# Optimization experiments

Hardware: AMD Instinct MI355X
Metric: run time of the kernel (lower is better)

The kernel has to match this reference:

```python
import jax, jax.numpy as jnp
import numpy as np

NUM_DOMAINS = 8
MARGIN = 1.0


def setup_inputs() -> dict:
    key = jax.random.key(0)
    k1, k2 = jax.random.split(key)
    features = jax.random.normal(k1, (4096, 1024), dtype=jnp.float32)
    domain_labels = jax.random.randint(k2, (4096,), 0, NUM_DOMAINS)
    return {"features": features, "domain_labels": domain_labels}


def reference(features, domain_labels):
    # Full BxB euclidean distance matrix (matches torch.cdist p=2, which uses
    # the mm-based path for this size). Safe sqrt so diagonal zeros are exact.
    sq = jnp.sum(features * features, axis=-1)                      # (B,)
    d2 = sq[:, None] + sq[None, :] - 2.0 * (features @ features.T)  # (B,B)
    d2 = jnp.maximum(d2, 0.0)
    dist = jnp.where(d2 > 0, jnp.sqrt(jnp.where(d2 > 0, d2, 1.0)), 0.0)
    vals = jax.nn.relu(MARGIN - dist)                               # (B,B)

    # Per-domain pair sums via one-hot contraction: s_d = m_d^T V m_d.
    onehot = (domain_labels[:, None] == jnp.arange(NUM_DOMAINS)[None, :]
              ).astype(features.dtype)                              # (B,K)
    n = onehot.sum(axis=0)                                          # (K,)
    row_sums = vals @ onehot                                        # (B,K)
    pair_sums = (onehot * row_sums).sum(axis=0)                     # (K,)

    valid = n > 1  # torch loop skips singleton domains
    per_domain = jnp.where(valid, pair_sums / jnp.maximum(n * n, 1.0), 0.0)
    cnt = valid.sum().astype(features.dtype)
    return jnp.where(cnt > 0, per_domain.sum() / jnp.maximum(cnt, 1.0), 0.0)
```

## Files before the change

### kernel.cpp

```cpp
#include <hip/hip_runtime.h>

#define NDOM 8
#define TT   32
#define KDIM 1024
#define RPAD 1040
#define BMAX 4096
#define GGRID 512

typedef float f32x4 __attribute__((ext_vector_type(4)));

__device__ inline void gload16(const void* g, void* l) {
    __builtin_amdgcn_global_load_lds(
        (const __attribute__((address_space(1))) unsigned int*)g,
        (__attribute__((address_space(3))) unsigned int*)l, 16, 0, 0);
}

__global__ __launch_bounds__(256) void k_prep(
    const float* __restrict__ F, const int* __restrict__ labels, int B,
    unsigned char* __restrict__ Fb, float* __restrict__ sq,
    int* __restrict__ perm, int* __restrict__ dom_off) {
    const int t = threadIdx.x, lane = t & 63, wv = t >> 6;

    if (blockIdx.x == 0) {
        __shared__ int lab[BMAX];
        __shared__ unsigned wcnt[4][NDOM];
        for (int i = t; i < BMAX; i += 256) lab[i] = (i < B) ? labels[i] : -1;
        __syncthreads();

        int nch = (B + 63) >> 6;
        int cpw = (nch + 3) >> 2;
        int c0 = wv * cpw, c1 = min(c0 + cpw, nch);
        unsigned long long below = (1ull << lane) - 1ull;

        unsigned cnt[NDOM];
#pragma unroll
        for (int d = 0; d < NDOM; ++d) cnt[d] = 0;
        for (int c = c0; c < c1; ++c) {
            int d = lab[c * 64 + lane];
#pragma unroll
            for (int dd = 0; dd < NDOM; ++dd)
                cnt[dd] += (unsigned)__popcll(__ballot(d == dd));
        }
        if (lane == 0)
#pragma unroll
            for (int dd = 0; dd < NDOM; ++dd) wcnt[wv][dd] = cnt[dd];
        __syncthreads();

        unsigned offs[NDOM + 1];
        offs[0] = 0;
#pragma unroll
        for (int dd = 0; dd < NDOM; ++dd)
            offs[dd + 1] = offs[dd] + wcnt[0][dd] + wcnt[1][dd] + wcnt[2][dd] + wcnt[3][dd];
        if (t <= NDOM) dom_off[t] = (int)offs[t];

        unsigned run[NDOM];
#pragma unroll
        for (int dd = 0; dd < NDOM; ++dd) {
            unsigned base = offs[dd];
            for (int w = 0; w < 4; ++w)
                if (w < wv) base += wcnt[w][dd];
            run[dd] = base;
        }
        for (int c = c0; c < c1; ++c) {
            int i = c * 64 + lane;
            int d = lab[i];
            int pos = -1;
#pragma unroll
            for (int dd = 0; dd < NDOM; ++dd) {
                unsigned long long m = __ballot(d == dd);
                if (d == dd) pos = (int)run[dd] + __popcll(m & below);
                run[dd] += (unsigned)__popcll(m);
            }
            if (i < B) perm[pos] = i;
        }
        return;
    }

    int i0 = (int)(blockIdx.x - 1) * 16;
    for (int j = wv; j < 16; j += 4) {
        int row = i0 + j;
        if (row >= B) break;
        const float4* srow = (const float4*)(F + (size_t)row * KDIM);
        int* drow = (int*)(Fb + (size_t)row * KDIM);
        float ss = 0.f;
#pragma unroll
        for (int it = 0; it < 4; ++it) {
            float4 v = srow[it * 64 + lane];
            ss += v.x * v.x + v.y * v.y + v.z * v.z + v.w * v.w;
            int p = __builtin_amdgcn_cvt_pk_fp8_f32(v.x, v.y, 0, false);
            p = __builtin_amdgcn_cvt_pk_fp8_f32(v.z, v.w, p, true);
            drow[it * 64 + lane] = p;
        }
#pragma unroll
        for (int s = 32; s > 0; s >>= 1) ss += __shfl_xor(ss, s);
        if (lane == 0) sq[row] = ss;
    }
}

__global__ __launch_bounds__(256) void k_gram(
    const unsigned char* __restrict__ Fb, const float* __restrict__ sq,
    const int* __restrict__ perm, const int* __restrict__ dom_off,
    float* __restrict__ part) {
    __shared__ __align__(16) unsigned char lA[TT * RPAD];
    __shared__ __align__(16) unsigned char lB[TT * RPAD];
    __shared__ int s_p[64];
    __shared__ float s_sq[64];
    __shared__ int s_offs[NDOM + 1], s_ts[NDOM + 1];
    __shared__ float s_ps[NDOM];

    const int t = threadIdx.x, lane = t & 63, wv = t >> 6;
    const int m16 = lane & 15, quad = lane >> 4;
    const int wm = (wv & 1) * 16, wn = (wv >> 1) * 16;

    if (t == 0) {
        int T = 0;
        for (int d = 0; d < NDOM; ++d) {
            int o0 = dom_off[d], o1 = dom_off[d + 1];
            s_offs[d] = o0;
            s_ts[d] = T;
            int n = o1 - o0;
            int nt = (n + TT - 1) / TT;
            T += nt * (nt + 1) / 2;
        }
        s_offs[NDOM] = dom_off[NDOM];
        s_ts[NDOM] = T;
    }
    if (t < NDOM) s_ps[t] = 0.f;
    __syncthreads();
    const int T = s_ts[NDOM];

    for (int tile = blockIdx.x; tile < T; tile += gridDim.x) {
        int dom = 0;
        while (tile >= s_ts[dom + 1]) ++dom;
        int off = s_offs[dom], n = s_offs[dom + 1] - off;
        int nt = (n + TT - 1) / TT;
        int rel = tile - s_ts[dom];
        int ty = 0, rem = rel;
        while (rem >= nt - ty) { rem -= nt - ty; ++ty; }
        int tx = ty + rem;
        int tr = ty * TT, tc = tx * TT;
        bool diag = (ty == tx);

        if (t < 64) {
            int r = (t < 32) ? min(tr + t, n - 1) : min(tc + (t - 32), n - 1);
            int p = perm[off + r];
            s_p[t] = p;
            s_sq[t] = sq[p];
        }
        __syncthreads();

#pragma unroll
        for (int j = 0; j < 16; ++j) {
            int r = wv * 16 + j;
            if (r < 32) {
                const unsigned char* g = Fb + (size_t)s_p[r] * KDIM + lane * 16;
                gload16(g, lA + r * RPAD);
            } else if (!diag) {
                const unsigned char* g = Fb + (size_t)s_p[r] * KDIM + lane * 16;
                gload16(g, lB + (r - 32) * RPAD);
            }
        }
        __syncthreads();

        const unsigned char* Bbuf = diag ? lA : lB;
        const unsigned char* pa = lA + (wm + m16) * RPAD + quad * 8;
        const unsigned char* pb = Bbuf + (wn + m16) * RPAD + quad * 8;
        f32x4 ac0 = (f32x4){0.f, 0.f, 0.f, 0.f};
        f32x4 ac1 = (f32x4){0.f, 0.f, 0.f, 0.f};
#pragma unroll
        for (int ks = 0; ks < 32; ks += 2) {
            long a0 = *(const long*)(pa + ks * 32);
            long b0 = *(const long*)(pb + ks * 32);
            long a1 = *(const long*)(pa + ks * 32 + 32);
            long b1 = *(const long*)(pb + ks * 32 + 32);
            ac0 = __builtin_amdgcn_mfma_f32_16x16x32_fp8_fp8(a0, b0, ac0, 0, 0, 0);
            ac1 = __builtin_amdgcn_mfma_f32_16x16x32_fp8_fp8(a1, b1, ac1, 0, 0, 0);
        }

        float local = 0.f;
        int lr0 = wm + quad * 4;
        int lc = wn + m16;
        int pc = tc + lc;
        if (pc < n) {
            float sb = s_sq[32 + lc];
#pragma unroll
            for (int r = 0; r < 4; ++r) {
                int pr = tr + lr0 + r;
                if (pr < n) {
                    float val;
                    if (pr == pc) {
                        val = 1.0f;
                    } else {
                        float d2 = s_sq[lr0 + r] + sb - 2.0f * (ac0[r] + ac1[r]);
                        d2 = fmaxf(d2, 0.f);
                        val = fmaxf(1.0f - sqrtf(d2), 0.f);
                    }
                    local += val;
                }
            }
        }
        if (!diag) local *= 2.f;
#pragma unroll
        for (int s = 32; s > 0; s >>= 1) local += __shfl_xor(local, s);
        if (lane == 0) atomicAdd(&s_ps[dom], local);
        __syncthreads();
    }

    __syncthreads();
    if (t < NDOM) part[blockIdx.x * NDOM + t] = s_ps[t];
}

__global__ __launch_bounds__(256) void k_final(
    const float* __restrict__ part, const int* __restrict__ dom_off,
    float* __restrict__ out) {
    __shared__ float red[8][32];
    int t = threadIdx.x;
    int d = t & 7, ch = t >> 3;
    float s = 0.f;
    for (int b = ch; b < GGRID; b += 32) s += part[b * NDOM + d];
    red[d][ch] = s;
    __syncthreads();
    if (t < NDOM) {
        float ps = 0.f;
#pragma unroll
        for (int c = 0; c < 32; ++c) ps += red[t][c];
        red[t][0] = ps;
    }
    __syncthreads();
    if (t == 0) {
        float acc = 0.f;
        int v = 0;
        for (int dd = 0; dd < NDOM; ++dd) {
            int n = dom_off[dd + 1] - dom_off[dd];
            if (n > 1) {
                acc += red[dd][0] / ((float)n * (float)n);
                ++v;
            }
        }
        out[0] = (v > 0) ? acc / (float)v : 0.f;
    }
}

extern "C" void kernel_launch(void* const* d_in, const int* in_sizes, int n_in,
                              void* d_out, int out_size, void* d_ws, size_t ws_size,
                              hipStream_t stream) {
    const float* F = (const float*)d_in[0];
    const int* labels = (const int*)d_in[1];
    int B = in_sizes[1];

    char* ws = (char*)d_ws;
    unsigned char* Fb = (unsigned char*)ws;
    float* sq = (float*)(ws + (size_t)BMAX * KDIM);
    int* perm = (int*)(ws + (size_t)BMAX * KDIM + BMAX * 4);
    int* dom_off = (int*)(ws + (size_t)BMAX * KDIM + BMAX * 8);
    float* part = (float*)(ws + (size_t)BMAX * KDIM + BMAX * 8 + 256);

    int ncv = (B + 15) / 16;
    k_prep<<<ncv + 1, 256, 0, stream>>>(F, labels, B, Fb, sq, perm, dom_off);
    k_gram<<<GGRID, 256, 0, stream>>>(Fb, sq, perm, dom_off, part);
    k_final<<<1, 256, 0, stream>>>(part, dom_off, (float*)d_out);
}
```

Measured before the change: 95.88 us.

## Fuse final reduction into gram kernel via last-block counter, prefetch tile indices

Removes the separate k_final launch. Each gram block publishes its per-domain partials, and the last block to arrive on an atomic counter (reset in k_prep) performs the final reduction. The perm and sq lookups for the next tile are prefetched into registers while the current tile's LDS loads are in flight, and k_prep now handles 8 rows per block instead of 16, doubling the number of conversion blocks. The costs are one extra atomic and fence per block, plus some reliance on the ordering of the atomic and memory fences for correctness.

```diff
diff --git a/kernel.cpp b/kernel.cpp
--- a/kernel.cpp
+++ b/kernel.cpp
@@ -18,7 +18,7 @@
 __global__ __launch_bounds__(256) void k_prep(
     const float* __restrict__ F, const int* __restrict__ labels, int B,
     unsigned char* __restrict__ Fb, float* __restrict__ sq,
-    int* __restrict__ perm, int* __restrict__ dom_off) {
+    int* __restrict__ perm, int* __restrict__ dom_off, unsigned* __restrict__ bar) {
     const int t = threadIdx.x, lane = t & 63, wv = t >> 6;
 
     if (blockIdx.x == 0) {
@@ -52,6 +52,7 @@
         for (int dd = 0; dd < NDOM; ++dd)
             offs[dd + 1] = offs[dd] + wcnt[0][dd] + wcnt[1][dd] + wcnt[2][dd] + wcnt[3][dd];
         if (t <= NDOM) dom_off[t] = (int)offs[t];
+        if (t == 0) *bar = 0u;
 
         unsigned run[NDOM];
 #pragma unroll
@@ -76,8 +77,8 @@
         return;
     }
 
-    int i0 = (int)(blockIdx.x - 1) * 16;
-    for (int j = wv; j < 16; j += 4) {
+    int i0 = (int)(blockIdx.x - 1) * 8;
+    for (int j = wv; j < 8; j += 4) {
         int row = i0 + j;
         if (row >= B) break;
         const float4* srow = (const float4*)(F + (size_t)row * KDIM);
@@ -100,13 +101,16 @@
 __global__ __launch_bounds__(256) void k_gram(
     const unsigned char* __restrict__ Fb, const float* __restrict__ sq,
     const int* __restrict__ perm, const int* __restrict__ dom_off,
-    float* __restrict__ part) {
+    float* __restrict__ part, unsigned* __restrict__ bar,
+    float* __restrict__ out) {
     __shared__ __align__(16) unsigned char lA[TT * RPAD];
     __shared__ __align__(16) unsigned char lB[TT * RPAD];
     __shared__ int s_p[64];
     __shared__ float s_sq[64];
     __shared__ int s_offs[NDOM + 1], s_ts[NDOM + 1];
     __shared__ float s_ps[NDOM];
+    __shared__ float red[NDOM][33];
+    __shared__ unsigned s_last;
 
     const int t = threadIdx.x, lane = t & 63, wv = t >> 6;
     const int m16 = lane & 15, quad = lane >> 4;
@@ -129,24 +133,42 @@
     __syncthreads();
     const int T = s_ts[NDOM];
 
-    for (int tile = blockIdx.x; tile < T; tile += gridDim.x) {
-        int dom = 0;
+    auto decode = [&](int tile, int& off, int& n, int& tr, int& tc,
+                      int& dom, bool& diag) {
+        dom = 0;
         while (tile >= s_ts[dom + 1]) ++dom;
-        int off = s_offs[dom], n = s_offs[dom + 1] - off;
+        off = s_offs[dom];
+        n = s_offs[dom + 1] - off;
         int nt = (n + TT - 1) / TT;
         int rel = tile - s_ts[dom];
         int ty = 0, rem = rel;
         while (rem >= nt - ty) { rem -= nt - ty; ++ty; }
         int tx = ty + rem;
-        int tr = ty * TT, tc = tx * TT;
-        bool diag = (ty == tx);
-
-        if (t < 64) {
+        tr = ty * TT;
+        tc = tx * TT;
+        diag = (ty == tx);
+    };
+
+    int pf_p = 0;
+    float pf_sq = 0.f;
+    auto prefetch = [&](int tile) {
+        if (tile < T && t < 64) {
+            int off, n, tr, tc, dom;
+            bool dg;
+            decode(tile, off, n, tr, tc, dom, dg);
             int r = (t < 32) ? min(tr + t, n - 1) : min(tc + (t - 32), n - 1);
-            int p = perm[off + r];
-            s_p[t] = p;
-            s_sq[t] = sq[p];
-        }
+            pf_p = perm[off + r];
+            pf_sq = sq[pf_p];
+        }
+    };
+    prefetch(blockIdx.x);
+
+    for (int tile = blockIdx.x; tile < T; tile += gridDim.x) {
+        int off, n, tr, tc, dom;
+        bool diag;
+        decode(tile, off, n, tr, tc, dom, diag);
+
+        if (t < 64) { s_p[t] = pf_p; s_sq[t] = pf_sq; }
         __syncthreads();
 
 #pragma unroll
@@ -160,6 +182,7 @@
                 gload16(g, lB + (r - 32) * RPAD);
             }
         }
+        prefetch(tile + (int)gridDim.x);
         __syncthreads();
 
         const unsigned char* Bbuf = diag ? lA : lB;
@@ -206,38 +229,40 @@
         __syncthreads();
     }
 
-    __syncthreads();
-    if (t < NDOM) part[blockIdx.x * NDOM + t] = s_ps[t];
-}
-
-__global__ __launch_bounds__(256) void k_final(
-    const float* __restrict__ part, const int* __restrict__ dom_off,
-    float* __restrict__ out) {
-    __shared__ float red[8][32];
-    int t = threadIdx.x;
-    int d = t & 7, ch = t >> 3;
-    float s = 0.f;
-    for (int b = ch; b < GGRID; b += 32) s += part[b * NDOM + d];
-    red[d][ch] = s;
-    __syncthreads();
-    if (t < NDOM) {
-        float ps = 0.f;
-#pragma unroll
-        for (int c = 0; c < 32; ++c) ps += red[t][c];
-        red[t][0] = ps;
-    }
+    if (t < NDOM)
+        __hip_atomic_store(&part[blockIdx.x * NDOM + t], s_ps[t],
+                           __ATOMIC_RELAXED, __HIP_MEMORY_SCOPE_AGENT);
     __syncthreads();
     if (t == 0) {
-        float acc = 0.f;
-        int v = 0;
-        for (int dd = 0; dd < NDOM; ++dd) {
-            int n = dom_off[dd + 1] - dom_off[dd];
-            if (n > 1) {
-                acc += red[dd][0] / ((float)n * (float)n);
-                ++v;
-            }
-        }
-        out[0] = (v > 0) ? acc / (float)v : 0.f;
+        __threadfence();
+        unsigned old = atomicAdd(bar, 1u);
+        s_last = (old == (unsigned)gridDim.x - 1) ? 1u : 0u;
+    }
+    __syncthreads();
+    if (s_last) {
+        if (t == 0) __threadfence();
+        __syncthreads();
+        int d = t & 7, ch = t >> 3;
+        float s = 0.f;
+        for (int b = ch; b < GGRID; b += 32)
+            s += __hip_atomic_load(&part[b * NDOM + d], __ATOMIC_RELAXED,
+                                   __HIP_MEMORY_SCOPE_AGENT);
+        red[d][ch] = s;
+        __syncthreads();
+        if (t == 0) {
+            float acc = 0.f;
+            int v = 0;
+            for (int dd = 0; dd < NDOM; ++dd) {
+                int n = s_offs[dd + 1] - s_offs[dd];
+                if (n > 1) {
+                    float ps = 0.f;
+                    for (int c = 0; c < 32; ++c) ps += red[dd][c];
+                    acc += ps / ((float)n * (float)n);
+                    ++v;
+                }
+            }
+            out[0] = (v > 0) ? acc / (float)v : 0.f;
+        }
     }
 }
 
@@ -253,10 +278,10 @@
     float* sq = (float*)(ws + (size_t)BMAX * KDIM);
     int* perm = (int*)(ws + (size_t)BMAX * KDIM + BMAX * 4);
     int* dom_off = (int*)(ws + (size_t)BMAX * KDIM + BMAX * 8);
+    unsigned* bar = (unsigned*)(ws + (size_t)BMAX * KDIM + BMAX * 8 + 128);
     float* part = (float*)(ws + (size_t)BMAX * KDIM + BMAX * 8 + 256);
 
-    int ncv = (B + 15) / 16;
-    k_prep<<<ncv + 1, 256, 0, stream>>>(F, labels, B, Fb, sq, perm, dom_off);
-    k_gram<<<GGRID, 256, 0, stream>>>(Fb, sq, perm, dom_off, part);
-    k_final<<<1, 256, 0, stream>>>(part, dom_off, (float*)d_out);
-}
+    int ncv = (B + 7) / 8;
+    k_prep<<<ncv + 1, 256, 0, stream>>>(F, labels, B, Fb, sq, perm, dom_off, bar);
+    k_gram<<<GGRID, 256, 0, stream>>>(Fb, sq, perm, dom_off, part, bar, (float*)d_out);
+}
```

Result: slower. 102.0 us (+6.3%).

## Enlarge gram tiles to 64x64 with 2x2 MFMA blocks per wave

Applied to the files above, without the earlier changes.

Doubles the tile edge from 32 to 64 rows, so each wave now computes a 32x32 sub-block with four fp8 MFMA accumulators. Each loaded A and B fragment is reused twice, and the tile count drops to about a quarter. LDS use per block roughly doubles to about 133KB, which may cut occupancy to one block per CU, and diagonal tiles waste more work. The final reduction kernel is also simplified by folding the per-domain sum into thread 0.

```diff
diff --git a/kernel.cpp b/kernel.cpp
--- a/kernel.cpp
+++ b/kernel.cpp
@@ -1,7 +1,7 @@
 #include <hip/hip_runtime.h>
 
 #define NDOM 8
-#define TT   32
+#define TT   64
 #define KDIM 1024
 #define RPAD 1040
 #define BMAX 4096
@@ -103,14 +103,14 @@
     float* __restrict__ part) {
     __shared__ __align__(16) unsigned char lA[TT * RPAD];
     __shared__ __align__(16) unsigned char lB[TT * RPAD];
-    __shared__ int s_p[64];
-    __shared__ float s_sq[64];
+    __shared__ int s_p[128];
+    __shared__ float s_sq[128];
     __shared__ int s_offs[NDOM + 1], s_ts[NDOM + 1];
     __shared__ float s_ps[NDOM];
 
     const int t = threadIdx.x, lane = t & 63, wv = t >> 6;
     const int m16 = lane & 15, quad = lane >> 4;
-    const int wm = (wv & 1) * 16, wn = (wv >> 1) * 16;
+    const int wm = (wv & 1) * 32, wn = (wv >> 1) * 32;
 
     if (t == 0) {
         int T = 0;
@@ -141,8 +141,8 @@
         int tr = ty * TT, tc = tx * TT;
         bool diag = (ty == tx);
 
-        if (t < 64) {
-            int r = (t < 32) ? min(tr + t, n - 1) : min(tc + (t - 32), n - 1);
+        if (t < 128) {
+            int r = (t < 64) ? min(tr + t, n - 1) : min(tc + (t - 64), n - 1);
             int p = perm[off + r];
             s_p[t] = p;
             s_sq[t] = sq[p];
@@ -152,50 +152,59 @@
 #pragma unroll
         for (int j = 0; j < 16; ++j) {
             int r = wv * 16 + j;
-            if (r < 32) {
-                const unsigned char* g = Fb + (size_t)s_p[r] * KDIM + lane * 16;
-                gload16(g, lA + r * RPAD);
-            } else if (!diag) {
-                const unsigned char* g = Fb + (size_t)s_p[r] * KDIM + lane * 16;
-                gload16(g, lB + (r - 32) * RPAD);
-            }
-        }
-        __syncthreads();
-
-        const unsigned char* Bbuf = diag ? lA : lB;
-        const unsigned char* pa = lA + (wm + m16) * RPAD + quad * 8;
-        const unsigned char* pb = Bbuf + (wn + m16) * RPAD + quad * 8;
-        f32x4 ac0 = (f32x4){0.f, 0.f, 0.f, 0.f};
-        f32x4 ac1 = (f32x4){0.f, 0.f, 0.f, 0.f};
-#pragma unroll
-        for (int ks = 0; ks < 32; ks += 2) {
-            long a0 = *(const long*)(pa + ks * 32);
-            long b0 = *(const long*)(pb + ks * 32);
-            long a1 = *(const long*)(pa + ks * 32 + 32);
-            long b1 = *(const long*)(pb + ks * 32 + 32);
-            ac0 = __builtin_amdgcn_mfma_f32_16x16x32_fp8_fp8(a0, b0, ac0, 0, 0, 0);
-            ac1 = __builtin_amdgcn_mfma_f32_16x16x32_fp8_fp8(a1, b1, ac1, 0, 0, 0);
+            gload16(Fb + (size_t)s_p[r] * KDIM + lane * 16, lA + r * RPAD);
+            if (!diag)
+                gload16(Fb + (size_t)s_p[64 + r] * KDIM + lane * 16, lB + r * RPAD);
+        }
+        __syncthreads();
+
+        const unsigned char* Bb = diag ? lA : lB;
+        const unsigned char* pa0 = lA + (wm + m16) * RPAD + quad * 8;
+        const unsigned char* pa1 = lA + (wm + 16 + m16) * RPAD + quad * 8;
+        const unsigned char* pb0 = Bb + (wn + m16) * RPAD + quad * 8;
+        const unsigned char* pb1 = Bb + (wn + 16 + m16) * RPAD + quad * 8;
+        f32x4 a00 = (f32x4){0.f, 0.f, 0.f, 0.f};
+        f32x4 a01 = (f32x4){0.f, 0.f, 0.f, 0.f};
+        f32x4 a10 = (f32x4){0.f, 0.f, 0.f, 0.f};
+        f32x4 a11 = (f32x4){0.f, 0.f, 0.f, 0.f};
+#pragma unroll
+        for (int ks = 0; ks < 32; ++ks) {
+            long av0 = *(const long*)(pa0 + ks * 32);
+            long av1 = *(const long*)(pa1 + ks * 32);
+            long bv0 = *(const long*)(pb0 + ks * 32);
+            long bv1 = *(const long*)(pb1 + ks * 32);
+            a00 = __builtin_amdgcn_mfma_f32_16x16x32_fp8_fp8(av0, bv0, a00, 0, 0, 0);
+            a01 = __builtin_amdgcn_mfma_f32_16x16x32_fp8_fp8(av0, bv1, a01, 0, 0, 0);
+            a10 = __builtin_amdgcn_mfma_f32_16x16x32_fp8_fp8(av1, bv0, a10, 0, 0, 0);
+            a11 = __builtin_amdgcn_mfma_f32_16x16x32_fp8_fp8(av1, bv1, a11, 0, 0, 0);
         }
 
         float local = 0.f;
-        int lr0 = wm + quad * 4;
-        int lc = wn + m16;
-        int pc = tc + lc;
-        if (pc < n) {
-            float sb = s_sq[32 + lc];
-#pragma unroll
-            for (int r = 0; r < 4; ++r) {
-                int pr = tr + lr0 + r;
-                if (pr < n) {
-                    float val;
-                    if (pr == pc) {
-                        val = 1.0f;
-                    } else {
-                        float d2 = s_sq[lr0 + r] + sb - 2.0f * (ac0[r] + ac1[r]);
-                        d2 = fmaxf(d2, 0.f);
-                        val = fmaxf(1.0f - sqrtf(d2), 0.f);
+#pragma unroll
+        for (int im = 0; im < 2; ++im) {
+            int lr0 = wm + im * 16 + quad * 4;
+#pragma unroll
+            for (int in = 0; in < 2; ++in) {
+                f32x4 av = (im == 0) ? ((in == 0) ? a00 : a01)
+                                     : ((in == 0) ? a10 : a11);
+                int lc = wn + in * 16 + m16;
+                int pc = tc + lc;
+                if (pc >= n) continue;
+                float sb = s_sq[64 + lc];
+#pragma unroll
+                for (int r = 0; r < 4; ++r) {
+                    int pr = tr + lr0 + r;
+                    if (pr < n) {
+                        float val;
+                        if (pr == pc) {
+                            val = 1.0f;
+                        } else {
+                            float d2 = s_sq[lr0 + r] + sb - 2.0f * av[r];
+                            d2 = fmaxf(d2, 0.f);
+                            val = fmaxf(1.0f - sqrtf(d2), 0.f);
+                        }
+                        local += val;
                     }
-                    local += val;
                 }
             }
         }
@@ -220,20 +229,15 @@
     for (int b = ch; b < GGRID; b += 32) s += part[b * NDOM + d];
     red[d][ch] = s;
     __syncthreads();
-    if (t < NDOM) {
-        float ps = 0.f;
-#pragma unroll
-        for (int c = 0; c < 32; ++c) ps += red[t][c];
-        red[t][0] = ps;
-    }
-    __syncthreads();
     if (t == 0) {
         float acc = 0.f;
         int v = 0;
         for (int dd = 0; dd < NDOM; ++dd) {
             int n = dom_off[dd + 1] - dom_off[dd];
             if (n > 1) {
-                acc += red[dd][0] / ((float)n * (float)n);
+                float ps = 0.f;
+                for (int c = 0; c < 32; ++c) ps += red[dd][c];
+                acc += ps / ((float)n * (float)n);
                 ++v;
             }
         }
```

New measurement: 97.78 us. Within noise of the previous version (+2.0%).
